# Kernel optimization log

Hardware: AMD Instinct MI355X
Metric: run time of the kernel (lower is better)

The kernel has to match this reference:

```python
import jax, jax.numpy as jnp
from jax import lax
import numpy as np

B, N, C = 32, 24564, 81
CENTER_VAR, SIZE_VAR = 0.1, 0.2
CONF_THRESH, IOU_THRESH = 0.01, 0.45
PRE_NMS_K, MAX_DET = 100, 100
EPS = 1e-8


def setup_inputs() -> dict:
    key = jax.random.key(0)
    k1, k2, k3, k4 = jax.random.split(key, 4)
    location_preds = jax.random.normal(k1, (B, N, 4), dtype=jnp.float32)
    confidence_preds = jax.random.normal(k2, (B, N, C), dtype=jnp.float32)
    # priors in center form (cx, cy, w, h), all in (0, 1), w/h in [0.05, 0.5]
    cxcy = jax.random.uniform(k3, (N, 2), dtype=jnp.float32)
    wh = 0.05 + 0.45 * jax.random.uniform(k4, (N, 2), dtype=jnp.float32)
    priors = jnp.concatenate([cxcy, wh], axis=-1)
    return {"location_preds": location_preds,
            "confidence_preds": confidence_preds,
            "priors": priors}


def _decode_corner(loc, priors):
    # loc: [B,N,4], priors: [N,4] center form -> corner-form boxes [B,N,4]
    cxcy = loc[..., :2] * CENTER_VAR * priors[None, :, 2:] + priors[None, :, :2]
    wh = jnp.exp(loc[..., 2:] * SIZE_VAR) * priors[None, :, 2:]
    return jnp.concatenate([cxcy - wh * 0.5, cxcy + wh * 0.5], axis=-1)


def _pairwise_iou(boxes):
    # boxes: [K,4] corner form -> [K,K]
    lt = jnp.maximum(boxes[:, None, :2], boxes[None, :, :2])
    rb = jnp.minimum(boxes[:, None, 2:], boxes[None, :, 2:])
    wh = jnp.clip(rb - lt, 0.0)
    inter = wh[..., 0] * wh[..., 1]
    area = jnp.prod(jnp.clip(boxes[:, 2:] - boxes[:, :2], 0.0), axis=-1)  # [K]
    return inter / (area[:, None] + area[None, :] - inter + EPS)


def _nms_one_class(boxes, scores):
    # boxes: [N,4], scores: [N] -> kept top-K boxes/scores for this class
    scores = jnp.where(scores > CONF_THRESH, scores, 0.0)
    top_s, idx = lax.top_k(scores, PRE_NMS_K)          # [K]
    top_b = boxes[idx]                                  # [K,4] sorted by score desc
    iou = _pairwise_iou(top_b)                          # [K,K]
    order = jnp.arange(PRE_NMS_K)

    def body(i, keep):
        suppressed = jnp.any(keep & (iou[:, i] > IOU_THRESH) & (order < i))
        return keep.at[i].set((top_s[i] > 0.0) & jnp.logical_not(suppressed))

    keep = lax.fori_loop(0, PRE_NMS_K, body, jnp.zeros(PRE_NMS_K, dtype=bool))
    return top_b, jnp.where(keep, top_s, 0.0)


def _per_image(boxes, scores):
    # boxes: [N,4], scores: [N,C]; class 0 is background
    cls_scores = scores[:, 1:].T                        # [C-1, N]
    b, s = jax.vmap(_nms_one_class, in_axes=(None, 0))(boxes, cls_scores)
    labels = jnp.broadcast_to(jnp.arange(1, C)[:, None], (C - 1, PRE_NMS_K))
    b = b.reshape(-1, 4)
    s = s.reshape(-1)
    labels = labels.reshape(-1)
    top_s, idx = lax.top_k(s, MAX_DET)
    return b[idx], top_s, labels[idx]


def reference(location_preds, confidence_preds, priors):
    scores = jax.nn.softmax(confidence_preds, axis=2)   # [B,N,C]
    bboxes = _decode_corner(location_preds, priors)     # [B,N,4]
    boxes_out, scores_out, labels_out = jax.vmap(_per_image)(bboxes, scores)
    # boxes_out [B,MAX_DET,4], scores_out [B,MAX_DET], labels_out [B,MAX_DET]
    return boxes_out, scores_out, labels_out
```

## Files before the change

kernel.cpp:

```cpp
#include <hip/hip_runtime.h>
#include <cstdint>
#include <cstddef>

#define BB 32
#define NN 24564
#define CC 81
#define CM1 80
#define KTOP 100
#define MAXDET 100
#define CBINS 28
#define CSHIFT 21
#define BASEBITS 0x3C000000u
#define SPECBITS 0x3D400000u
#define SPECPF   0.0468281f
#define CAP2 2048
#define CAPB 25
#define BPI 96
#define FCH 8
#define FCHN 1000
#define FPAD 1024
#define NCAND (CM1 * KTOP)

typedef unsigned long long ull;
typedef unsigned int uint;
typedef float floatx4 __attribute__((ext_vector_type(4)));
typedef floatx4 uf4 __attribute__((aligned(4)));

__global__ __launch_bounds__(256) void zero_kernel(uint* __restrict__ p, int nwords) {
    int i = blockIdx.x * 256 + threadIdx.x;
    if (i < nwords) p[i] = 0u;
}

__device__ __forceinline__ void bitonic_sort256(ull* a, int S, int tid) {
    for (int k = 2; k <= S; k <<= 1) {
        for (int j = k >> 1; j > 0; j >>= 1) {
            for (int i = tid; i < S; i += 256) {
                int ixj = i ^ j;
                if (ixj > i) {
                    ull x = a[i], y = a[ixj];
                    bool up = ((i & k) == 0);
                    if ((x > y) == up) { a[i] = y; a[ixj] = x; }
                }
            }
            __syncthreads();
        }
    }
}

__global__ __launch_bounds__(256) void softmax_spec_kernel(const float* __restrict__ conf,
                                                           float2* __restrict__ mxs,
                                                           ull* __restrict__ cand,
                                                           uint* __restrict__ ccnt,
                                                           uint* __restrict__ ovf) {
    __shared__ ull  sbuf[CM1 * CAPB];
    __shared__ uint scnt[CM1];
    int tid = threadIdx.x;
    if (tid < CM1) scnt[tid] = 0u;
    __syncthreads();

    int b = blockIdx.x / BPI, j = blockIdx.x % BPI;
    int n = j * 256 + tid;
    if (n < NN) {
        const float* row = conf + ((size_t)b * NN + n) * CC;
        const uf4* row4 = reinterpret_cast<const uf4*>(row);
        float r[CC];
        #pragma unroll
        for (int q = 0; q < 20; ++q) {
            floatx4 v = row4[q];
            r[4 * q] = v.x; r[4 * q + 1] = v.y; r[4 * q + 2] = v.z; r[4 * q + 3] = v.w;
        }
        r[80] = row[80];

        float mx = r[0];
        #pragma unroll
        for (int c = 1; c < CC; ++c) mx = fmaxf(mx, r[c]);

        float s = 0.f;
        #pragma unroll
        for (int c = 0; c < CC; ++c) {
            r[c] = expf(__fsub_rn(r[c], mx));
            s = __fadd_rn(s, r[c]);
        }
        mxs[(size_t)b * NN + n] = make_float2(mx, s);

        float rcp = __builtin_amdgcn_rcpf(s);
        uint nn = (uint)n;
        #pragma unroll
        for (int c = 1; c < CC; ++c) {
            float p = __fmul_rn(r[c], rcp);
            if (p > SPECPF) {
                float sc = __fdiv_rn(r[c], s);
                uint eb = __float_as_uint(sc);
                if (eb >= SPECBITS) {
                    uint pp = atomicAdd(&scnt[c - 1], 1u);
                    if (pp < CAPB) sbuf[(c - 1) * CAPB + pp] = (((ull)(~eb)) << 32) | nn;
                }
            }
        }
    }
    __syncthreads();

    if (tid < CM1) {
        uint c2 = scnt[tid];
        if (c2) {
            int bc = b * CM1 + tid;
            uint nstore = c2 > CAPB ? CAPB : c2;
            uint base = atomicAdd(ccnt + bc, nstore);
            if (c2 > CAPB || base + nstore > CAP2) ovf[bc] = 1u;
            uint lim = base + nstore; if (lim > CAP2) lim = CAP2;
            for (uint i = 0; base + i < lim; ++i)
                cand[(size_t)bc * CAP2 + base + i] = sbuf[tid * CAPB + i];
        }
    }
}

__global__ __launch_bounds__(256) void nms_kernel(const ull* __restrict__ cand,
                                                  const uint* __restrict__ ccnt,
                                                  const uint* __restrict__ ovf,
                                                  const float* __restrict__ conf,
                                                  const float2* __restrict__ mxs,
                                                  const float* __restrict__ loc,
                                                  const float* __restrict__ priors,
                                                  float* __restrict__ nms_scores,
                                                  float* __restrict__ nms_boxes) {
    int bc = blockIdx.x;
    int bimg = bc / CM1, ccls = bc % CM1;
    __shared__ ull arr2[CAP2];
    __shared__ ull keysort[KTOP];
    __shared__ uint hist[CBINS];
    __shared__ uint s_cut, s_cnt2;
    __shared__ float bx[KTOP][4];
    __shared__ float sv[KTOP];
    __shared__ ull mlo[KTOP], mhi[KTOP];
    __shared__ ull keeplo, keephi;

    int tid = threadIdx.x;
    for (int i = tid; i < CBINS; i += 256) hist[i] = 0u;
    if (tid < KTOP) keysort[tid] = ((ull)0xFFFFFFFFu) << 32;
    if (tid == 0) { s_cut = 0u; s_cnt2 = 0u; }
    __syncthreads();

    uint rawcnt = ccnt[bc];
    bool flagged = !(ovf[bc] == 0u && rawcnt >= (uint)KTOP);

    if (!flagged) {
        int cc = (int)rawcnt; if (cc > CAP2) cc = CAP2;
        const ull* crow = cand + (size_t)bc * CAP2;
        for (int i = tid; i < cc; i += 256) {
            uint bits = ~(uint)(crow[i] >> 32);
            uint bin = (bits - BASEBITS) >> CSHIFT;
            if (bin >= CBINS) bin = CBINS - 1;
            atomicAdd(&hist[bin], 1u);
        }
        __syncthreads();
        if (tid == 0) {
            uint Kt = (uint)(cc < KTOP ? cc : KTOP);
            uint cum = 0; int bb2 = 0;
            for (int i = CBINS - 1; i >= 0; --i) {
                cum += hist[i];
                if (cum >= Kt) { bb2 = i; break; }
            }
            s_cut = BASEBITS + ((uint)bb2 << CSHIFT);
        }
        __syncthreads();
        uint cutv = s_cut;
        for (int i = tid; i < cc; i += 256) {
            ull k = crow[i];
            uint bits = ~(uint)(k >> 32);
            if (bits >= cutv) { uint p = atomicAdd(&s_cnt2, 1u); arr2[p] = k; }
        }
        __syncthreads();
    } else {
        int c = ccls + 1;
        for (int n = tid; n < NN; n += 256) {
            float x = conf[((size_t)bimg * NN + n) * CC + c];
            float2 ms = mxs[(size_t)bimg * NN + n];
            float e = expf(__fsub_rn(x, ms.x));
            float sc = __fdiv_rn(e, ms.y);
            if (sc > 0.01f) {
                uint bits = __float_as_uint(sc);
                uint bin = (bits - BASEBITS) >> CSHIFT;
                if (bin >= CBINS) bin = CBINS - 1;
                atomicAdd(&hist[bin], 1u);
            }
        }
        __syncthreads();
        if (tid == 0) {
            uint total = 0;
            for (int i = 0; i < CBINS; ++i) total += hist[i];
            uint Kt = total < KTOP ? total : KTOP;
            s_cut = 0xFFFFFFFFu;
            if (Kt > 0) {
                uint cum = 0; int bb2 = 0;
                for (int i = CBINS - 1; i >= 0; --i) {
                    cum += hist[i];
                    if (cum >= Kt) { bb2 = i; break; }
                }
                uint cutbin = (cum <= CAP2) ? (uint)bb2 : (uint)(bb2 + 1);
                s_cut = BASEBITS + (cutbin << CSHIFT);
            }
        }
        __syncthreads();
        uint cutv = s_cut;
        for (int n = tid; n < NN; n += 256) {
            float x = conf[((size_t)bimg * NN + n) * CC + c];
            float2 ms = mxs[(size_t)bimg * NN + n];
            float e = expf(__fsub_rn(x, ms.x));
            float sc = __fdiv_rn(e, ms.y);
            if (sc > 0.01f) {
                uint bits = __float_as_uint(sc);
                if (bits >= cutv) {
                    uint p = atomicAdd(&s_cnt2, 1u);
                    if (p < CAP2) arr2[p] = (((ull)(~bits)) << 32) | (uint)n;
                }
            }
        }
        __syncthreads();
    }

    int scc = (int)s_cnt2; if (scc > CAP2) scc = CAP2;

    {
        ull myk[8]; int rnk[8];
        #pragma unroll
        for (int t = 0; t < 8; ++t) {
            int i = tid + t * 256;
            myk[t] = (i < scc) ? arr2[i] : ~0ull;
            rnk[t] = 0;
        }
        for (int j = 0; j < scc; ++j) {
            ull kj = arr2[j];
            #pragma unroll
            for (int t = 0; t < 8; ++t) rnk[t] += (kj < myk[t]) ? 1 : 0;
        }
        #pragma unroll
        for (int t = 0; t < 8; ++t) {
            int i = tid + t * 256;
            if (i < scc && rnk[t] < KTOP) keysort[rnk[t]] = myk[t];
        }
    }
    __syncthreads();

    if (tid < KTOP) {
        ull kk = keysort[tid];
        float val = __uint_as_float(~(uint)(kk >> 32));
        uint n = (uint)(kk & 0xFFFFFFFFu);
        sv[tid] = val;
        float4 l = reinterpret_cast<const float4*>(loc)[(size_t)bimg * NN + n];
        float4 p = reinterpret_cast<const float4*>(priors)[n];
        float cx = __fadd_rn(__fmul_rn(__fmul_rn(l.x, 0.1f), p.z), p.x);
        float cy = __fadd_rn(__fmul_rn(__fmul_rn(l.y, 0.1f), p.w), p.y);
        float w  = __fmul_rn(expf(__fmul_rn(l.z, 0.2f)), p.z);
        float h  = __fmul_rn(expf(__fmul_rn(l.w, 0.2f)), p.w);
        bx[tid][0] = __fsub_rn(cx, __fmul_rn(w, 0.5f));
        bx[tid][1] = __fsub_rn(cy, __fmul_rn(h, 0.5f));
        bx[tid][2] = __fadd_rn(cx, __fmul_rn(w, 0.5f));
        bx[tid][3] = __fadd_rn(cy, __fmul_rn(h, 0.5f));
    }
    __syncthreads();

    if (tid < KTOP) {
        float x1 = bx[tid][0], y1 = bx[tid][1], x2 = bx[tid][2], y2 = bx[tid][3];
        float ai = __fmul_rn(fmaxf(__fsub_rn(x2, x1), 0.f), fmaxf(__fsub_rn(y2, y1), 0.f));
        ull lo = 0, hi = 0;
        for (int jj = 0; jj < KTOP; ++jj) {
            float jx1 = bx[jj][0], jy1 = bx[jj][1], jx2 = bx[jj][2], jy2 = bx[jj][3];
            float iw = fmaxf(__fsub_rn(fminf(x2, jx2), fmaxf(x1, jx1)), 0.f);
            float ih = fmaxf(__fsub_rn(fminf(y2, jy2), fmaxf(y1, jy1)), 0.f);
            float inter = __fmul_rn(iw, ih);
            float aj = __fmul_rn(fmaxf(__fsub_rn(jx2, jx1), 0.f), fmaxf(__fsub_rn(jy2, jy1), 0.f));
            float denom = __fadd_rn(__fsub_rn(__fadd_rn(ai, aj), inter), 1e-8f);
            float iou = __fdiv_rn(inter, denom);
            if (iou > 0.45f) { if (jj < 64) lo |= (1ull << jj); else hi |= (1ull << (jj - 64)); }
        }
        mlo[tid] = lo; mhi[tid] = hi;
    }
    __syncthreads();

    if (tid == 0) {
        ull klo = 0, khi = 0;
        for (int i = 0; i < KTOP; ++i) {
            ull sup = (mlo[i] & klo) | (mhi[i] & khi);
            bool kp = (sv[i] > 0.f) && (sup == 0ull);
            if (kp) { if (i < 64) klo |= (1ull << i); else khi |= (1ull << (i - 64)); }
        }
        keeplo = klo; keephi = khi;
    }
    __syncthreads();

    if (tid < KTOP) {
        bool kp = (tid < 64) ? ((keeplo >> tid) & 1ull) : ((keephi >> (tid - 64)) & 1ull);
        size_t obase = (size_t)bc * KTOP + tid;
        nms_scores[obase] = kp ? sv[tid] : 0.f;
        float4 o; o.x = bx[tid][0]; o.y = bx[tid][1]; o.z = bx[tid][2]; o.w = bx[tid][3];
        reinterpret_cast<float4*>(nms_boxes)[obase] = o;
    }
}

__global__ __launch_bounds__(256) void final_topk_kernel(const float* __restrict__ nms_scores,
                                                         const float* __restrict__ nms_boxes,
                                                         float* __restrict__ out) {
    int b = blockIdx.x;
    __shared__ ull arr[CAP2];
    __shared__ ull arr2[FPAD];
    __shared__ uint hist[CBINS];
    __shared__ uint s_cut, s_mode, s_cnt2, s_nz;
    int tid = threadIdx.x;

    const float* srow = nms_scores + (size_t)b * NCAND;
    for (int i = tid; i < CBINS; i += 256) hist[i] = 0u;
    if (tid == 0) { s_cut = 0u; s_mode = 0u; s_cnt2 = 0u; s_nz = 0u; }
    __syncthreads();

    uint mynz = 0;
    for (int i = tid; i < NCAND; i += 256) {
        float s = srow[i];
        if (s > 0.f) {
            ++mynz;
            uint bits = __float_as_uint(s);
            uint bin = (bits - BASEBITS) >> CSHIFT;
            if (bin >= CBINS) bin = CBINS - 1;
            atomicAdd(&hist[bin], 1u);
        }
    }
    if (mynz) atomicAdd(&s_nz, mynz);
    __syncthreads();
    if (tid == 0) {
        if (s_nz >= (uint)KTOP) {
            uint cum = 0; int bb2 = 0;
            for (int i = CBINS - 1; i >= 0; --i) {
                cum += hist[i];
                if (cum >= (uint)KTOP) { bb2 = i; break; }
            }
            if (cum <= CAP2) { s_cut = BASEBITS + ((uint)bb2 << CSHIFT); s_mode = 1u; }
        }
    }
    __syncthreads();

    if (s_mode) {
        uint cutv = s_cut;
        for (int i = tid; i < NCAND; i += 256) {
            float s = srow[i];
            if (s > 0.f) {
                uint bits = __float_as_uint(s);
                if (bits >= cutv) {
                    uint p = atomicAdd(&s_cnt2, 1u);
                    arr[p] = (((ull)(~bits)) << 32) | (uint)i;
                }
            }
        }
        __syncthreads();
        int fcc = (int)s_cnt2;
        int FS = 1; while (FS < fcc) FS <<= 1; if (FS < 2) FS = 2;
        for (int i = fcc + tid; i < FS; i += 256) arr[i] = ~0ull;
        __syncthreads();
        bitonic_sort256(arr, FS, tid);
    } else {
        for (int ch = 0; ch < FCH; ++ch) {
            for (int i = tid; i < FPAD; i += 256) {
                ull key;
                if (i < FCHN) {
                    float s = srow[ch * FCHN + i];
                    uint bits = (s > 0.f) ? __float_as_uint(s) : 0u;
                    key = (((ull)(~bits)) << 32) | (uint)(ch * FCHN + i);
                } else key = ~0ull;
                arr2[i] = key;
            }
            __syncthreads();
            bitonic_sort256(arr2, FPAD, tid);
            if (tid < KTOP) arr[ch * KTOP + tid] = arr2[tid];
            __syncthreads();
        }
        for (int i = FCH * KTOP + tid; i < FPAD; i += 256) arr[i] = ~0ull;
        __syncthreads();
        bitonic_sort256(arr, FPAD, tid);
    }

    if (tid < MAXDET) {
        ull kk = arr[tid];
        uint hb = (uint)(kk >> 32);
        uint idx = (uint)(kk & 0xFFFFFFFFu);
        float val = __uint_as_float(~hb);
        float4 b4 = reinterpret_cast<const float4*>(nms_boxes)[(size_t)b * NCAND + idx];
        reinterpret_cast<float4*>(out)[(size_t)b * MAXDET + tid] = b4;
        out[BB * MAXDET * 4 + b * MAXDET + tid] = val;
        out[BB * MAXDET * 5 + b * MAXDET + tid] = (float)(idx / KTOP + 1);
    }
}

extern "C" void kernel_launch(void* const* d_in, const int* in_sizes, int n_in,
                              void* d_out, int out_size, void* d_ws, size_t ws_size,
                              hipStream_t stream) {
    const float* loc    = (const float*)d_in[0];
    const float* conf   = (const float*)d_in[1];
    const float* priors = (const float*)d_in[2];
    float* out = (float*)d_out;

    char* ws = (char*)d_ws;
    float* nms_scores = (float*)ws;
    float* nms_boxes  = nms_scores + (size_t)BB * CM1 * KTOP;
    ull*   cand       = (ull*)(nms_boxes + (size_t)BB * CM1 * KTOP * 4);
    float2* mxs       = (float2*)(cand + (size_t)BB * CM1 * CAP2);
    uint*  ccnt       = (uint*)(mxs + (size_t)BB * NN);
    uint*  ovf        = ccnt + (size_t)BB * CM1;

    zero_kernel<<<(BB * CM1 * 2 + 255) / 256, 256, 0, stream>>>(ccnt, BB * CM1 * 2);

    softmax_spec_kernel<<<BB * BPI, 256, 0, stream>>>(conf, mxs, cand, ccnt, ovf);
    nms_kernel<<<BB * CM1, 256, 0, stream>>>(cand, ccnt, ovf, conf, mxs, loc, priors,
                                             nms_scores, nms_boxes);
    final_topk_kernel<<<BB, 256, 0, stream>>>(nms_scores, nms_boxes, out);
}
```

Before: 232.6 us.

## Stage softmax rows through LDS with async global-to-LDS loads and a logit threshold

The softmax/speculation kernel now runs 64-thread blocks that bulk-copy a contiguous 64-row tile into LDS with global_load_lds 16-byte transfers. Before, each thread did strided per-row vector loads that coalesce poorly. Exps are no longer kept in registers: each candidate is pre-filtered by comparing its raw logit against mx+log(s)+const, and exp is recomputed only for the few that pass. This cuts register pressure and exp work, at the cost of LDS-bank-conflicted row reads, a smaller per-block candidate buffer, and a log-domain threshold that could misclassify borderline scores.

Result: slower. 364.7 us (+56.8%).

```diff
diff --git a/kernel.cpp b/kernel.cpp
--- a/kernel.cpp
+++ b/kernel.cpp
@@ -12,10 +12,10 @@
 #define CSHIFT 21
 #define BASEBITS 0x3C000000u
 #define SPECBITS 0x3D400000u
-#define SPECPF   0.0468281f
+#define L_SP (-3.0612707f)
 #define CAP2 2048
-#define CAPB 25
-#define BPI 96
+#define CAPB2 12
+#define SBPI 384
 #define FCH 8
 #define FCHN 1000
 #define FPAD 1024
@@ -23,12 +23,17 @@
 
 typedef unsigned long long ull;
 typedef unsigned int uint;
-typedef float floatx4 __attribute__((ext_vector_type(4)));
-typedef floatx4 uf4 __attribute__((aligned(4)));
 
 __global__ __launch_bounds__(256) void zero_kernel(uint* __restrict__ p, int nwords) {
     int i = blockIdx.x * 256 + threadIdx.x;
     if (i < nwords) p[i] = 0u;
+}
+
+__device__ __forceinline__ void gload16(const void* g, void* l) {
+    __builtin_amdgcn_global_load_lds(
+        (const __attribute__((address_space(1))) unsigned int*)g,
+        (__attribute__((address_space(3))) unsigned int*)l,
+        16, 0, 0);
 }
 
 __device__ __forceinline__ void bitonic_sort256(ull* a, int S, int tid) {
@@ -47,69 +52,70 @@
     }
 }
 
-__global__ __launch_bounds__(256) void softmax_spec_kernel(const float* __restrict__ conf,
-                                                           float2* __restrict__ mxs,
-                                                           ull* __restrict__ cand,
-                                                           uint* __restrict__ ccnt,
-                                                           uint* __restrict__ ovf) {
-    __shared__ ull  sbuf[CM1 * CAPB];
+__global__ __launch_bounds__(64) void softmax_spec_kernel(const float* __restrict__ conf,
+                                                          float2* __restrict__ mxs,
+                                                          ull* __restrict__ cand,
+                                                          uint* __restrict__ ccnt,
+                                                          uint* __restrict__ ovf) {
+    __shared__ __align__(16) float tile[64 * CC];
+    __shared__ ull  sbuf[CM1 * CAPB2];
     __shared__ uint scnt[CM1];
     int tid = threadIdx.x;
-    if (tid < CM1) scnt[tid] = 0u;
-    __syncthreads();
-
-    int b = blockIdx.x / BPI, j = blockIdx.x % BPI;
-    int n = j * 256 + tid;
+    for (int c = tid; c < CM1; c += 64) scnt[c] = 0u;
+
+    int b = blockIdx.x / SBPI, j = blockIdx.x % SBPI;
+    int n0 = j * 64;
+    int rows = NN - n0; if (rows > 64) rows = 64;
+    int bytes = rows * (CC * 4);
+    const char* gsrc = (const char*)(conf + ((size_t)b * NN + n0) * CC);
+    char* ltile = (char*)tile;
+    #pragma unroll
+    for (int it = 0; it < 21; ++it) {
+        int o = it * 1024 + tid * 16;
+        if (o < bytes) gload16(gsrc + o, ltile + it * 1024);
+    }
+    __syncthreads();
+
+    int n = n0 + tid;
     if (n < NN) {
-        const float* row = conf + ((size_t)b * NN + n) * CC;
-        const uf4* row4 = reinterpret_cast<const uf4*>(row);
-        float r[CC];
+        const float* row = tile + tid * CC;
+        float mx = row[0];
         #pragma unroll
-        for (int q = 0; q < 20; ++q) {
-            floatx4 v = row4[q];
-            r[4 * q] = v.x; r[4 * q + 1] = v.y; r[4 * q + 2] = v.z; r[4 * q + 3] = v.w;
-        }
-        r[80] = row[80];
-
-        float mx = r[0];
-        #pragma unroll
-        for (int c = 1; c < CC; ++c) mx = fmaxf(mx, r[c]);
+        for (int c = 1; c < CC; ++c) mx = fmaxf(mx, row[c]);
 
         float s = 0.f;
         #pragma unroll
-        for (int c = 0; c < CC; ++c) {
-            r[c] = expf(__fsub_rn(r[c], mx));
-            s = __fadd_rn(s, r[c]);
-        }
+        for (int c = 0; c < CC; ++c) s = __fadd_rn(s, expf(__fsub_rn(row[c], mx)));
         mxs[(size_t)b * NN + n] = make_float2(mx, s);
 
-        float rcp = __builtin_amdgcn_rcpf(s);
+        float Tsp = mx + __logf(s) + L_SP;
         uint nn = (uint)n;
         #pragma unroll
         for (int c = 1; c < CC; ++c) {
-            float p = __fmul_rn(r[c], rcp);
-            if (p > SPECPF) {
-                float sc = __fdiv_rn(r[c], s);
+            float x = row[c];
+            if (x > Tsp) {
+                float e = expf(__fsub_rn(x, mx));
+                float sc = __fdiv_rn(e, s);
                 uint eb = __float_as_uint(sc);
                 if (eb >= SPECBITS) {
                     uint pp = atomicAdd(&scnt[c - 1], 1u);
-                    if (pp < CAPB) sbuf[(c - 1) * CAPB + pp] = (((ull)(~eb)) << 32) | nn;
+                    if (pp < CAPB2) sbuf[(c - 1) * CAPB2 + pp] = (((ull)(~eb)) << 32) | nn;
                 }
             }
         }
     }
     __syncthreads();
 
-    if (tid < CM1) {
-        uint c2 = scnt[tid];
+    for (int c = tid; c < CM1; c += 64) {
+        uint c2 = scnt[c];
         if (c2) {
-            int bc = b * CM1 + tid;
-            uint nstore = c2 > CAPB ? CAPB : c2;
+            int bc = b * CM1 + c;
+            uint nstore = c2 > CAPB2 ? CAPB2 : c2;
             uint base = atomicAdd(ccnt + bc, nstore);
-            if (c2 > CAPB || base + nstore > CAP2) ovf[bc] = 1u;
+            if (c2 > CAPB2 || base + nstore > CAP2) ovf[bc] = 1u;
             uint lim = base + nstore; if (lim > CAP2) lim = CAP2;
             for (uint i = 0; base + i < lim; ++i)
-                cand[(size_t)bc * CAP2 + base + i] = sbuf[tid * CAPB + i];
+                cand[(size_t)bc * CAP2 + base + i] = sbuf[c * CAPB2 + i];
         }
     }
 }
@@ -406,7 +412,7 @@
 
     zero_kernel<<<(BB * CM1 * 2 + 255) / 256, 256, 0, stream>>>(ccnt, BB * CM1 * 2);
 
-    softmax_spec_kernel<<<BB * BPI, 256, 0, stream>>>(conf, mxs, cand, ccnt, ovf);
+    softmax_spec_kernel<<<BB * SBPI, 64, 0, stream>>>(conf, mxs, cand, ccnt, ovf);
     nms_kernel<<<BB * CM1, 256, 0, stream>>>(cand, ccnt, ovf, conf, mxs, loc, priors,
                                              nms_scores, nms_boxes);
     final_topk_kernel<<<BB, 256, 0, stream>>>(nms_scores, nms_boxes, out);
```
